# Kernel optimization log

Measured on AMD Instinct MI355X. Metric: run time of the kernel, lower is better.

## Reference

```python
import jax, jax.numpy as jnp
import numpy as np

N, D, H, C, E, I, L, B = 16000, 128, 2, 128, 256000, 512, 2, 64
NTYPES = 10


def setup_inputs() -> dict:
    key = jax.random.key(0)
    ks = jax.random.split(key, 20)
    s = 0.05
    inp = {
        'x': jax.random.normal(ks[0], (N, D), jnp.float32),
        'hetro_emb': jax.random.normal(ks[1], (NTYPES, D), jnp.float32) * s,
        'Wq': jax.random.normal(ks[2], (D, H * C), jnp.float32) * s,
        'bq': jnp.zeros((H * C,), jnp.float32),
        'Wk': jax.random.normal(ks[3], (D, H * C), jnp.float32) * s,
        'bk': jnp.zeros((H * C,), jnp.float32),
        'Wv': jax.random.normal(ks[4], (D, H * C), jnp.float32) * s,
        'bv': jnp.zeros((H * C,), jnp.float32),
        'We': jax.random.normal(ks[5], (D, H * C), jnp.float32) * s,
        'Wskip': jax.random.normal(ks[6], (D, C), jnp.float32) * s,
        'bskip': jnp.zeros((C,), jnp.float32),
        'ln_gamma': jnp.ones((L, D), jnp.float32),
        'ln_beta': jnp.zeros((L, D), jnp.float32),
        'ffn_w1': jax.random.normal(ks[7], (L, D, I), jnp.float32) * s,
        'ffn_b1': jnp.zeros((L, I), jnp.float32),
        'ffn_w2': jax.random.normal(ks[8], (L, I, D), jnp.float32) * s,
        'ffn_b2': jnp.zeros((L, D), jnp.float32),
        'edge_index': jax.random.randint(ks[9], (2, E), 0, N, jnp.int64),
        'edge_type': jax.random.randint(ks[10], (E,), 0, NTYPES, jnp.int64),
        'mask_idx': jax.random.randint(ks[11], (B,), 0, N, jnp.int64),
    }
    return inp


def _layer_norm(h, gamma, beta, eps=1e-6):
    mu = h.mean(-1, keepdims=True)
    var = ((h - mu) ** 2).mean(-1, keepdims=True)
    return (h - mu) * jax.lax.rsqrt(var + eps) * gamma + beta


def reference(x, hetro_emb, Wq, bq, Wk, bk, Wv, bv, We, Wskip, bskip,
              ln_gamma, ln_beta, ffn_w1, ffn_b1, ffn_w2, ffn_b2,
              edge_index, edge_type, mask_idx):
    src, dst = edge_index[0], edge_index[1]  # messages flow src(j) -> dst(i)
    edge_attr_raw = hetro_emb[edge_type]     # [E, D], computed once outside the layer loop
    scale = 1.0 / jnp.sqrt(jnp.asarray(C, x.dtype))

    h = x
    pre = h
    for l in range(L):
        # shared GRANConv weights across layers (same module appended n_gcn_layer times)
        q = (h @ Wq + bq).reshape(-1, H, C)
        k = (h @ Wk + bk).reshape(-1, H, C)
        v = (h @ Wv + bv).reshape(-1, H, C)
        eproj = (edge_attr_raw @ We).reshape(-1, H, C)  # [E, H, C]
        kj = k[src] + eproj                              # [E, H, C]
        logits = (q[dst] * kj).sum(-1) * scale           # [E, H]
        # segment softmax over destination nodes
        m = jax.ops.segment_max(logits, dst, num_segments=N)  # [N, H]
        a = jnp.exp(logits - m[dst])
        ssum = jax.ops.segment_sum(a, dst, num_segments=N)
        alpha = a / (ssum[dst] + 1e-16)                  # [E, H]
        msg = (v[src] + eproj) * alpha[..., None]        # [E, H, C]
        agg = jax.ops.segment_sum(msg, dst, num_segments=N)  # [N, H, C]
        out = agg.mean(1) + (h @ Wskip + bskip)          # concat=False -> head mean; root skip
        # residual + LN + FFN (no activation between the two FFN linears)
        hres = out + pre
        hln = _layer_norm(hres, ln_gamma[l], ln_beta[l])
        h = (hln @ ffn_w1[l] + ffn_b1[l]) @ ffn_w2[l] + ffn_b2[l]
        pre = h

    return h[mask_idx]  # [B, D]
```

## Files before the change

### kernel.cpp

```cpp
#include <hip/hip_runtime.h>
#include <hip/hip_bf16.h>
#include <math.h>

#define DD 128
#define QW 896
#define NB 125
#define BCAP 4096

typedef _Float16 f16x8 __attribute__((ext_vector_type(8)));
typedef _Float16 f16x4 __attribute__((ext_vector_type(4)));
typedef _Float16 f16x2 __attribute__((ext_vector_type(2)));
typedef float f32x4 __attribute__((ext_vector_type(4)));

__device__ __forceinline__ float fdot2f(f16x2 a, f16x2 b, float c) {
#if __has_builtin(__builtin_amdgcn_fdot2)
  return __builtin_amdgcn_fdot2(a, b, c, false);
#else
  return fmaf((float)a[0], (float)b[0], fmaf((float)a[1], (float)b[1], c));
#endif
}

__global__ __launch_bounds__(256) void csr_count(const int* __restrict__ edst,
                                                 int* __restrict__ bparts, int E) {
  __shared__ int h[NB];
  const int tid = threadIdx.x;
  if (tid < NB) h[tid] = 0;
  __syncthreads();
  const int e0 = blockIdx.x * 2048;
  for (int k = 0; k < 8; ++k) {
    int e = e0 + k * 256 + tid;
    if (e < E) atomicAdd(&h[edst[e] >> 7], 1);
  }
  __syncthreads();
  if (tid < 128) bparts[blockIdx.x * 128 + tid] = (tid < NB) ? h[tid] : 0;
}

__global__ __launch_bounds__(128) void csr_scan(const int* __restrict__ bparts, int nblk,
                                                int* __restrict__ bbase,
                                                int* __restrict__ bcursor,
                                                int* __restrict__ offs, int E, int Nn) {
  __shared__ int sc[128];
  const int tid = threadIdx.x;
  int s = 0;
  for (int b = 0; b < nblk; ++b) s += bparts[b * 128 + tid];
  sc[tid] = (tid < NB) ? s : 0;
  __syncthreads();
  for (int d = 1; d < 128; d <<= 1) {
    int t = (tid >= d) ? sc[tid - d] : 0;
    __syncthreads();
    sc[tid] += t;
    __syncthreads();
  }
  const int excl = tid ? sc[tid - 1] : 0;
  if (tid < NB) { bbase[tid] = excl; bcursor[tid] = excl; }
  if (tid == 0) { bbase[NB] = E; offs[Nn] = E; }
}

__global__ __launch_bounds__(256) void csr_scatter(const int* __restrict__ edst,
                                                   const int* __restrict__ esrc,
                                                   const int* __restrict__ etyp,
                                                   int* __restrict__ bcursor,
                                                   unsigned* __restrict__ ebuf, int E) {
  __shared__ int h[NB], cur[NB];
  const int tid = threadIdx.x;
  if (tid < NB) h[tid] = 0;
  __syncthreads();
  const int e0 = blockIdx.x * 2048;
  int dd[8];
  for (int k = 0; k < 8; ++k) {
    int e = e0 + k * 256 + tid;
    dd[k] = (e < E) ? edst[e] : -1;
    if (dd[k] >= 0) atomicAdd(&h[dd[k] >> 7], 1);
  }
  __syncthreads();
  if (tid < NB && h[tid]) cur[tid] = atomicAdd(&bcursor[tid], h[tid]);
  __syncthreads();
  for (int k = 0; k < 8; ++k) {
    int e = e0 + k * 256 + tid;
    if (dd[k] >= 0) {
      int pos = atomicAdd(&cur[dd[k] >> 7], 1);
      ebuf[pos] = (unsigned)esrc[e] | ((unsigned)etyp[e] << 14) |
                  ((unsigned)(dd[k] & 127) << 18);
    }
  }
}

__global__ __launch_bounds__(256) void csr_fine(const unsigned* __restrict__ ebuf,
                                                const int* __restrict__ bbase,
                                                unsigned* __restrict__ epk,
                                                int* __restrict__ offs,
                                                int* __restrict__ dparts) {
  __shared__ unsigned sed[BCAP];
  __shared__ unsigned sout[BCAP];
  __shared__ int fh[128], sc[128], fc[128], hb[64];
  const int b = blockIdx.x, tid = threadIdx.x;
  const int base = bbase[b], cnt = bbase[b + 1] - base;
  for (int idx = tid; idx < cnt; idx += 256) sed[idx] = ebuf[base + idx];
  if (tid < 128) fh[tid] = 0;
  if (tid < 64) hb[tid] = 0;
  __syncthreads();
  for (int idx = tid; idx < cnt; idx += 256) atomicAdd(&fh[(sed[idx] >> 18) & 127], 1);
  __syncthreads();
  if (tid < 128) sc[tid] = fh[tid];
  __syncthreads();
  for (int d = 1; d < 128; d <<= 1) {
    int t = (tid < 128 && tid >= d) ? sc[tid - d] : 0;
    __syncthreads();
    if (tid < 128) sc[tid] += t;
    __syncthreads();
  }
  if (tid < 128) {
    const int excl = tid ? sc[tid - 1] : 0;
    offs[b * 128 + tid] = base + excl;
    fc[tid] = excl;
    atomicAdd(&hb[min(fh[tid], 63)], 1);
  }
  __syncthreads();
  if (tid < 64) dparts[b * 64 + tid] = hb[tid];
  for (int idx = tid; idx < cnt; idx += 256) {
    const unsigned v = sed[idx];
    const int pos = atomicAdd(&fc[(v >> 18) & 127], 1);
    sout[pos] = (v & 0x3FFF) | (((v >> 14) & 0xF) << 18);
  }
  __syncthreads();
  for (int idx = tid; idx < cnt; idx += 256) epk[base + idx] = sout[idx];
}

__global__ __launch_bounds__(64) void deg_scan(const int* __restrict__ dparts, int nblk,
                                               int* __restrict__ dcur) {
  __shared__ int tot[64];
  const int t = threadIdx.x;
  int s = 0;
  for (int b = 0; b < nblk; ++b) s += dparts[b * 64 + t];
  tot[t] = s;
  __syncthreads();
  int acc = 0;
  for (int d = t + 1; d < 64; ++d) acc += tot[d];
  dcur[t] = acc;
}

__global__ __launch_bounds__(256) void deg_order(const int* __restrict__ offs,
                                                 int* __restrict__ dcur,
                                                 int* __restrict__ order, int Nn) {
  __shared__ int h[64], cbase[64];
  const int tid = threadIdx.x;
  const int i = blockIdx.x * 256 + tid;
  if (tid < 64) h[tid] = 0;
  __syncthreads();
  int bk = -1;
  if (i < Nn) {
    bk = min(offs[i + 1] - offs[i], 63);
    atomicAdd(&h[bk], 1);
  }
  __syncthreads();
  if (tid < 64) {
    const int c = h[tid];
    cbase[tid] = c ? atomicAdd(&dcur[tid], c) : 0;
    h[tid] = 0;
  }
  __syncthreads();
  if (bk >= 0) {
    const int pos = cbase[bk] + atomicAdd(&h[bk], 1);
    order[pos] = i;
  }
}

__global__ __launch_bounds__(256) void pp_cast(
    const float* __restrict__ Wq, const float* __restrict__ Wk,
    const float* __restrict__ Wv, const float* __restrict__ Wsk,
    const float* __restrict__ bq, const float* __restrict__ bk,
    const float* __restrict__ bv, const float* __restrict__ bsk,
    const float* __restrict__ hemb, const float* __restrict__ We,
    const float* __restrict__ x,
    const float* __restrict__ fw1, const float* __restrict__ fb1,
    const float* __restrict__ fw2, const float* __restrict__ fb2,
    _Float16* __restrict__ WcatT, float* __restrict__ Wcat, float* __restrict__ bcat,
    _Float16* __restrict__ epth, _Float16* __restrict__ xh,
    _Float16* __restrict__ fw1h, _Float16* __restrict__ fw2Th,
    float* __restrict__ bfv, float* __restrict__ bzero, int Nn, int nb0) {
  __shared__ _Float16 tile[64][65];
  if (blockIdx.x >= nb0) {
    const int tb = blockIdx.x - nb0;
    const int l = tb >> 4, r2 = tb & 15;
    const int k0 = (r2 >> 1) << 6, j0 = (r2 & 1) << 6;
    const size_t base = (size_t)l * 65536;
    const int tid = threadIdx.x;
    for (int idx = tid; idx < 4096; idx += 256) {
      int rr = idx >> 6, cc = idx & 63;
      tile[rr][cc] = (_Float16)fw2[base + (size_t)(k0 + rr) * 128 + j0 + cc];
    }
    __syncthreads();
    for (int idx = tid; idx < 4096; idx += 256) {
      int rr = idx >> 6, cc = idx & 63;
      fw2Th[base + (size_t)(j0 + rr) * 512 + k0 + cc] = tile[cc][rr];
    }
    return;
  }
  int t = blockIdx.x * 256 + threadIdx.x;
  if (t < 256) {
    int l = t >> 7, j = t & 127;
    const float* b1 = fb1 + l * 512;
    const float* w2 = fw2 + (size_t)l * 65536 + j;
    float s0 = fb2[l * 128 + j], s1 = 0.f, s2 = 0.f, s3 = 0.f;
    for (int k = 0; k < 512; k += 4) {
      s0 = fmaf(b1[k], w2[(size_t)k * 128], s0);
      s1 = fmaf(b1[k + 1], w2[(size_t)(k + 1) * 128], s1);
      s2 = fmaf(b1[k + 2], w2[(size_t)(k + 2) * 128], s2);
      s3 = fmaf(b1[k + 3], w2[(size_t)(k + 3) * 128], s3);
    }
    bfv[t] = ((s0 + s1) + (s2 + s3));
    return;
  }
  t -= 256;
  if (t < 2560) {
    int ty = t >> 8, col = t & 255;
    float s0 = 0.f, s1 = 0.f, s2 = 0.f, s3 = 0.f;
    const float* hr = hemb + ty * 128;
    for (int c = 0; c < 128; c += 4) {
      s0 = fmaf(hr[c], We[c * 256 + col], s0);
      s1 = fmaf(hr[c + 1], We[(c + 1) * 256 + col], s1);
      s2 = fmaf(hr[c + 2], We[(c + 2) * 256 + col], s2);
      s3 = fmaf(hr[c + 3], We[(c + 3) * 256 + col], s3);
    }
    epth[t] = (_Float16)((s0 + s1) + (s2 + s3));
    return;
  }
  t -= 2560;
  if (t < 114688) {
    int n = t >> 7, k = t & 127;
    float v;
    if (n < 256) v = Wq[k * 256 + n];
    else if (n < 512) v = Wk[k * 256 + (n - 256)];
    else if (n < 768) v = Wv[k * 256 + (n - 512)];
    else v = Wsk[k * 128 + (n - 768)];
    WcatT[t] = (_Float16)v;
    Wcat[k * 896 + n] = v;
    return;
  }
  t -= 114688;
  if (t < 896) {
    float v;
    if (t < 256) v = bq[t];
    else if (t < 512) v = bk[t - 256];
    else if (t < 768) v = bv[t - 512];
    else v = bsk[t - 768];
    bcat[t] = v;
    return;
  }
  t -= 896;
  if (t < 1024) { bzero[t] = 0.f; return; }
  t -= 1024;
  if (t < 16384) {
    float4 v0 = *reinterpret_cast<const float4*>(fw1 + (size_t)t * 8);
    float4 v1 = *reinterpret_cast<const float4*>(fw1 + (size_t)t * 8 + 4);
    f16x8 o;
    o[0] = (_Float16)v0.x; o[1] = (_Float16)v0.y; o[2] = (_Float16)v0.z; o[3] = (_Float16)v0.w;
    o[4] = (_Float16)v1.x; o[5] = (_Float16)v1.y; o[6] = (_Float16)v1.z; o[7] = (_Float16)v1.w;
    *reinterpret_cast<f16x8*>(fw1h + (size_t)t * 8) = o;
    return;
  }
  t -= 16384;
  if (t < Nn * 16) {
    float4 v0 = *reinterpret_cast<const float4*>(x + (size_t)t * 8);
    float4 v1 = *reinterpret_cast<const float4*>(x + (size_t)t * 8 + 4);
    f16x8 o;
    o[0] = (_Float16)v0.x; o[1] = (_Float16)v0.y; o[2] = (_Float16)v0.z; o[3] = (_Float16)v0.w;
    o[4] = (_Float16)v1.x; o[5] = (_Float16)v1.y; o[6] = (_Float16)v1.z; o[7] = (_Float16)v1.w;
    *reinterpret_cast<f16x8*>(xh + (size_t)t * 8) = o;
  }
}

__global__ __launch_bounds__(256) void pp_bmid(const float* __restrict__ bfv,
                                               const float* __restrict__ Wcat,
                                               const float* __restrict__ bcat,
                                               float* __restrict__ bmid) {
  int t = blockIdx.x * 256 + threadIdx.x;
  if (t >= 1024) return;
  if (t < 128) { bmid[t] = bfv[t]; return; }
  int n = t - 128;
  float s0 = bcat[n], s1 = 0.f, s2 = 0.f, s3 = 0.f;
  for (int c = 0; c < 128; c += 4) {
    s0 = fmaf(bfv[c], Wcat[c * 896 + n], s0);
    s1 = fmaf(bfv[c + 1], Wcat[(c + 1) * 896 + n], s1);
    s2 = fmaf(bfv[c + 2], Wcat[(c + 2) * 896 + n], s2);
    s3 = fmaf(bfv[c + 3], Wcat[(c + 3) * 896 + n], s3);
  }
  bmid[t] = ((s0 + s1) + (s2 + s3));
}

__global__ __launch_bounds__(256) void wf_gemm(const _Float16* __restrict__ fw1h,
                                               const _Float16* __restrict__ fw2Th,
                                               float* __restrict__ Wf,
                                               _Float16* __restrict__ Wfh,
                                               _Float16* __restrict__ BtMid0) {
  const int z = blockIdx.z;
  const _Float16* A = fw1h + z * 65536;
  const _Float16* Bt = fw2Th + z * 65536;
  const int tid = threadIdx.x;
  const int wid = tid >> 6, lane = tid & 63;
  const int wr = wid >> 1, wc = wid & 1;
  const int il = lane & 15, g = lane >> 4;
  const int row0 = wr * 64, col0 = wc * 64;
  const _Float16* Ap = A + (size_t)(row0 + il) * 512 + 8 * g;
  const _Float16* Bp = Bt + (size_t)(col0 + il) * 512 + 8 * g;
  f32x4 acc[4][4];
#pragma unroll
  for (int a = 0; a < 4; ++a)
#pragma unroll
    for (int b = 0; b < 4; ++b) acc[a][b] = (f32x4){0.f, 0.f, 0.f, 0.f};
  for (int k0 = 0; k0 < 512; k0 += 32) {
    f16x8 af[4], bf[4];
#pragma unroll
    for (int f = 0; f < 4; ++f) {
      af[f] = *reinterpret_cast<const f16x8*>(Ap + (size_t)(f * 16) * 512 + k0);
      bf[f] = *reinterpret_cast<const f16x8*>(Bp + (size_t)(f * 16) * 512 + k0);
    }
#pragma unroll
    for (int fi = 0; fi < 4; ++fi)
#pragma unroll
      for (int fj = 0; fj < 4; ++fj)
        acc[fi][fj] = __builtin_amdgcn_mfma_f32_16x16x32_f16(af[fi], bf[fj], acc[fi][fj], 0, 0, 0);
  }
#pragma unroll
  for (int fj = 0; fj < 4; ++fj) {
    const int col = col0 + fj * 16 + il;
#pragma unroll
    for (int fi = 0; fi < 4; ++fi) {
#pragma unroll
      for (int i = 0; i < 4; ++i) {
        const int row = row0 + fi * 16 + g * 4 + i;
        const float v = acc[fi][fj][i];
        Wf[z * 16384 + row * 128 + col] = v;
        if (z == 0) {
          Wfh[row * 128 + col] = (_Float16)v;
          BtMid0[col * 128 + row] = (_Float16)v;
        }
      }
    }
  }
}

template <bool HAS_CFH, bool HAS_CH, bool HAS_CHT>
__global__ __launch_bounds__(256) void gemm_tn_f16(const _Float16* __restrict__ A,
                                                   const _Float16* __restrict__ Bt,
                                                   const float* __restrict__ bias,
                                                   _Float16* __restrict__ Cfh, int NF,
                                                   _Float16* __restrict__ Ch, int choff, int ldh,
                                                   _Float16* __restrict__ ChT, int ldt,
                                                   int M, int N, int K) {
  __shared__ __align__(16) char smA[32768];
  __shared__ __align__(16) char smB[32768];
  const int tid = threadIdx.x;
  const int wid = tid >> 6, lane = tid & 63;
  const int wr = wid >> 1, wc = wid & 1;
  const int il = lane & 15, g = lane >> 4;
  const int row0 = blockIdx.y * 128;
  const int col0 = blockIdx.x * 128;
  {
    const f16x8* Ag = reinterpret_cast<const f16x8*>(A + (size_t)row0 * 128);
    const f16x8* Bg = reinterpret_cast<const f16x8*>(Bt + (size_t)col0 * 128);
#pragma unroll
    for (int it = 0; it < 8; ++it) {
      const int c = it * 256 + tid;
      const int r = c >> 4;
      const int off = r * 256 + (((c & 15) << 4) ^ ((r & 7) << 4));
      f16x8 va = Ag[c];
      f16x8 vb = Bg[c];
      *reinterpret_cast<f16x8*>(smA + off) = va;
      *reinterpret_cast<f16x8*>(smB + off) = vb;
    }
  }
  __syncthreads();
  f32x4 acc[4][4];
#pragma unroll
  for (int a = 0; a < 4; ++a)
#pragma unroll
    for (int b = 0; b < 4; ++b) acc[a][b] = (f32x4){0.f, 0.f, 0.f, 0.f};
#pragma unroll
  for (int ks = 0; ks < 4; ++ks) {
    const int kb = ks * 64 + g * 16;
    f16x8 af[4], bf[4];
#pragma unroll
    for (int f = 0; f < 4; ++f) {
      const int ra = wr * 64 + f * 16 + il;
      const int rb = wc * 64 + f * 16 + il;
      af[f] = *reinterpret_cast<const f16x8*>(smA + ra * 256 + (kb ^ ((ra & 7) << 4)));
      bf[f] = *reinterpret_cast<const f16x8*>(smB + rb * 256 + (kb ^ ((rb & 7) << 4)));
    }
#pragma unroll
    for (int fi = 0; fi < 4; ++fi)
#pragma unroll
      for (int fj = 0; fj < 4; ++fj)
        acc[fi][fj] = __builtin_amdgcn_mfma_f32_16x16x32_f16(bf[fj], af[fi], acc[fi][fj], 0, 0, 0);
  }
#pragma unroll
  for (int fi = 0; fi < 4; ++fi) {
    const int row = row0 + wr * 64 + fi * 16 + il;
#pragma unroll
    for (int fj = 0; fj < 4; ++fj) {
      const int col = col0 + wc * 64 + fj * 16 + g * 4;
      const float4 b4 = *reinterpret_cast<const float4*>(bias + col);
      f16x4 o;
      o[0] = (_Float16)(acc[fi][fj][0] + b4.x);
      o[1] = (_Float16)(acc[fi][fj][1] + b4.y);
      o[2] = (_Float16)(acc[fi][fj][2] + b4.z);
      o[3] = (_Float16)(acc[fi][fj][3] + b4.w);
      if constexpr (HAS_CFH) {
        if (col < NF) *reinterpret_cast<f16x4*>(&Cfh[(size_t)row * NF + col]) = o;
      }
      if constexpr (HAS_CH) {
        if (col >= choff) *reinterpret_cast<f16x4*>(&Ch[(size_t)row * ldh + (col - choff)]) = o;
      }
      if constexpr (HAS_CHT) {
#pragma unroll
        for (int i = 0; i < 4; ++i) ChT[(size_t)(col + i) * ldt + row] = o[i];
      }
    }
  }
}

__global__ __launch_bounds__(256) void node_attn_ln_kernel(
    const _Float16* __restrict__ QKVSh, const _Float16* __restrict__ epth,
    const _Float16* __restrict__ hpre,
    const int* __restrict__ offs, const unsigned* __restrict__ epk,
    const int* __restrict__ order,
    const float* __restrict__ gamma, const float* __restrict__ beta,
    _Float16* __restrict__ hlnh, int Nn) {
  __shared__ float sqe[4][2][10];
  __shared__ __align__(16) _Float16 elds[2560];
  const int tid = threadIdx.x;
  for (int t = tid; t < 1280; t += 256)
    reinterpret_cast<unsigned*>(elds)[t] = reinterpret_cast<const unsigned*>(epth)[t];
  __syncthreads();
  const int w = tid >> 6, lane = tid & 63;
  const int i = order[blockIdx.x * 4 + w];
  const int sub = lane >> 5;
  const int r = lane & 31;
  const int half = r >> 4;
  const int co = r << 3;
  const float scale = 0.08838834764831845f;
  f16x8 qh = *reinterpret_cast<const f16x8*>(QKVSh + (size_t)i * QW + co);
  const f16x2* q2 = reinterpret_cast<const f16x2*>(&qh);
#pragma unroll
  for (int ty = 0; ty < 10; ++ty) {
    f16x8 ev = *reinterpret_cast<const f16x8*>(elds + (ty << 8) + co);
    const f16x2* e2 = reinterpret_cast<const f16x2*>(&ev);
    float s = 0.f;
#pragma unroll
    for (int p2 = 0; p2 < 4; ++p2) s = fdot2f(q2[p2], e2[p2], s);
    s += __shfl_xor(s, 1); s += __shfl_xor(s, 2);
    s += __shfl_xor(s, 4); s += __shfl_xor(s, 8);
    if (lane < 32 && (r & 15) == 0) sqe[w][half][ty] = s * scale;
  }
  __threadfence_block();
  float m_me = -1e30f, s_me = 0.f;
  float acc[8] = {0.f};
  const int ebeg = offs[i], eend = offs[i + 1];
  if (ebeg < eend) {
    const int last = eend - 1;
    unsigned pk0 = epk[min(ebeg + sub, last)];
    unsigned pk1 = epk[min(ebeg + 2 + sub, last)];
    const _Float16* r0p = QKVSh + (size_t)(pk0 & 0x3FFFF) * QW;
    const _Float16* r1p = QKVSh + (size_t)(pk1 & 0x3FFFF) * QW;
    f16x8 kv0 = *reinterpret_cast<const f16x8*>(r0p + 256 + co);
    f16x8 vv0 = *reinterpret_cast<const f16x8*>(r0p + 512 + co);
    f16x8 kv1 = *reinterpret_cast<const f16x8*>(r1p + 256 + co);
    f16x8 vv1 = *reinterpret_cast<const f16x8*>(r1p + 512 + co);
    for (int j = ebeg; j < eend; j += 2) {
      f16x8 kc = kv0, vc = vv0;
      const unsigned pkc = pk0;
      kv0 = kv1; vv0 = vv1; pk0 = pk1;
      pk1 = epk[min(j + 4 + sub, last)];
      const _Float16* rp = QKVSh + (size_t)(pk1 & 0x3FFFF) * QW;
      kv1 = *reinterpret_cast<const f16x8*>(rp + 256 + co);
      vv1 = *reinterpret_cast<const f16x8*>(rp + 512 + co);
      const int tyc = pkc >> 18;
      const f16x2* k2 = reinterpret_cast<const f16x2*>(&kc);
      float d = 0.f;
#pragma unroll
      for (int p2 = 0; p2 < 4; ++p2) d = fdot2f(q2[p2], k2[p2], d);
      d += __shfl_xor(d, 1); d += __shfl_xor(d, 2);
      d += __shfl_xor(d, 4); d += __shfl_xor(d, 8);
      d = d * scale + sqe[w][half][tyc];
      float e;
      if (d > m_me + 8.f) {
        const float rr = __expf(m_me - d);
        s_me *= rr;
#pragma unroll
        for (int t = 0; t < 8; ++t) acc[t] *= rr;
        m_me = d;
        e = 1.f;
      } else {
        e = __expf(d - m_me);
      }
      if (j + sub >= eend) e = 0.f;
      s_me += e;
      f16x8 ec = *reinterpret_cast<const f16x8*>(elds + (tyc << 8) + co);
      f16x8 ve = vc + ec;
#pragma unroll
      for (int t = 0; t < 8; ++t) acc[t] = fmaf((float)ve[t], e, acc[t]);
    }
  }
  const float mo = __shfl_xor(m_me, 32);
  const float so = __shfl_xor(s_me, 32);
  const float mf = fmaxf(m_me, mo);
  const float sc_me = __expf(m_me - mf);
  const float sc_o = __expf(mo - mf);
  const float s_tot = s_me * sc_me + so * sc_o;
  const float invme = 1.f / (s_tot + 1e-16f);
  float g[8];
#pragma unroll
  for (int t = 0; t < 8; ++t) {
    const float ao = __shfl_xor(acc[t], 32);
    const float a = (acc[t] * sc_me + ao * sc_o) * invme;
    g[t] = 0.5f * (a + __shfl_xor(a, 16));
  }
  const int cm = (r & 15) << 3;
  f16x8 sk = *reinterpret_cast<const f16x8*>(QKVSh + (size_t)i * QW + 768 + cm);
  f16x8 pr = *reinterpret_cast<const f16x8*>(hpre + (size_t)i * DD + cm);
  float xv[8];
#pragma unroll
  for (int t = 0; t < 8; ++t) xv[t] = g[t] + (float)sk[t] + (float)pr[t];
  float sm = 0.f;
#pragma unroll
  for (int t = 0; t < 8; ++t) sm += xv[t];
  sm += __shfl_xor(sm, 1); sm += __shfl_xor(sm, 2);
  sm += __shfl_xor(sm, 4); sm += __shfl_xor(sm, 8);
  const float mu = sm * (1.f / 128.f);
  float dx[8], vvs = 0.f;
#pragma unroll
  for (int t = 0; t < 8; ++t) { dx[t] = xv[t] - mu; vvs += dx[t] * dx[t]; }
  vvs += __shfl_xor(vvs, 1); vvs += __shfl_xor(vvs, 2);
  vvs += __shfl_xor(vvs, 4); vvs += __shfl_xor(vvs, 8);
  const float rstd = rsqrtf(vvs * (1.f / 128.f) + 1e-6f);
  if (lane < 16) {
    float4 gm0 = *reinterpret_cast<const float4*>(gamma + cm);
    float4 gm1 = *reinterpret_cast<const float4*>(gamma + cm + 4);
    float4 bt0 = *reinterpret_cast<const float4*>(beta + cm);
    float4 bt1 = *reinterpret_cast<const float4*>(beta + cm + 4);
    f16x8 o;
    o[0] = (_Float16)(dx[0] * rstd * gm0.x + bt0.x);
    o[1] = (_Float16)(dx[1] * rstd * gm0.y + bt0.y);
    o[2] = (_Float16)(dx[2] * rstd * gm0.z + bt0.z);
    o[3] = (_Float16)(dx[3] * rstd * gm0.w + bt0.w);
    o[4] = (_Float16)(dx[4] * rstd * gm1.x + bt1.x);
    o[5] = (_Float16)(dx[5] * rstd * gm1.y + bt1.y);
    o[6] = (_Float16)(dx[6] * rstd * gm1.z + bt1.z);
    o[7] = (_Float16)(dx[7] * rstd * gm1.w + bt1.w);
    *reinterpret_cast<f16x8*>(hlnh + (size_t)i * DD + cm) = o;
  }
}

__global__ __launch_bounds__(128) void final_kernel(const _Float16* __restrict__ hlnh1,
                                                    const float* __restrict__ Wf,
                                                    const float* __restrict__ bfv,
                                                    const int* __restrict__ midx,
                                                    float* __restrict__ out) {
  __shared__ float rowv[128];
  const int b = blockIdx.x, j = threadIdx.x;
  const int row = midx[b];
  rowv[j] = (float)hlnh1[(size_t)row * DD + j];
  __syncthreads();
  const float* w1 = Wf + 16384 + j;
  float s = bfv[128 + j];
#pragma unroll 4
  for (int c = 0; c < 128; ++c) s = fmaf(rowv[c], w1[c * 128], s);
  out[b * DD + j] = s;
}

extern "C" void kernel_launch(void* const* d_in, const int* in_sizes, int n_in,
                              void* d_out, int out_size, void* d_ws, size_t ws_size,
                              hipStream_t stream) {
  const float* x    = (const float*)d_in[0];
  const float* hemb = (const float*)d_in[1];
  const float* Wq   = (const float*)d_in[2];
  const float* bq   = (const float*)d_in[3];
  const float* Wk   = (const float*)d_in[4];
  const float* bk   = (const float*)d_in[5];
  const float* Wv   = (const float*)d_in[6];
  const float* bv   = (const float*)d_in[7];
  const float* We   = (const float*)d_in[8];
  const float* Wsk  = (const float*)d_in[9];
  const float* bsk  = (const float*)d_in[10];
  const float* lng  = (const float*)d_in[11];
  const float* lnb  = (const float*)d_in[12];
  const float* fw1  = (const float*)d_in[13];
  const float* fb1  = (const float*)d_in[14];
  const float* fw2  = (const float*)d_in[15];
  const float* fb2  = (const float*)d_in[16];
  const int* eidx   = (const int*)d_in[17];
  const int* etyp   = (const int*)d_in[18];
  const int* midx   = (const int*)d_in[19];

  const int Nn = in_sizes[0] / DD;
  const int E = in_sizes[18];

  const int* esrc = eidx;
  const int* edst = eidx + E;

  char* p = (char*)d_ws;
  auto alloc = [&](size_t bytes) -> void* {
    void* r = (void*)p;
    p += (bytes + 255) & ~(size_t)255;
    return r;
  };
  _Float16* QKVSh = (_Float16*)alloc((size_t)Nn * QW * 2);
  _Float16* xh    = (_Float16*)alloc((size_t)Nn * DD * 2);
  _Float16* hln0  = (_Float16*)alloc((size_t)Nn * DD * 2);
  _Float16* hln1  = (_Float16*)alloc((size_t)Nn * DD * 2);
  _Float16* h1h   = (_Float16*)alloc((size_t)Nn * DD * 2);
  _Float16* WcatT = (_Float16*)alloc((size_t)QW * DD * 2);
  float*    Wcat  = (float*)alloc((size_t)DD * QW * 4);
  float*    bcat  = (float*)alloc(QW * 4);
  _Float16* epth  = (_Float16*)alloc(2560 * 2);
  _Float16* fw1h  = (_Float16*)alloc((size_t)2 * DD * 512 * 2);
  _Float16* fw2Th = (_Float16*)alloc((size_t)2 * DD * 512 * 2);
  float*    Wf    = (float*)alloc(2 * 128 * 128 * 4);
  _Float16* Wfh   = (_Float16*)alloc(128 * 128 * 2);
  float*    bfv   = (float*)alloc(256 * 4);
  float*    bzero = (float*)alloc(1024 * 4);
  _Float16* BtMid = (_Float16*)alloc((size_t)1024 * 128 * 2);
  float*    bmid  = (float*)alloc(1024 * 4);
  int* offs   = (int*)alloc((size_t)(Nn + 1) * 4);
  int* bbase  = (int*)alloc((NB + 1) * 4);
  int* bcursor= (int*)alloc((NB + 1) * 4);
  int* dcur   = (int*)alloc(64 * 4);
  int* order  = (int*)alloc((size_t)Nn * 4);
  const int nsblk = (E + 2047) / 2048;
  int* bparts = (int*)alloc((size_t)nsblk * 128 * 4);
  int* dparts = (int*)alloc((size_t)NB * 64 * 4);
  unsigned* ebuf = (unsigned*)alloc((size_t)E * 4);
  unsigned* epk  = (unsigned*)alloc((size_t)E * 4);

  csr_count<<<nsblk, 256, 0, stream>>>(edst, bparts, E);
  csr_scan<<<1, 128, 0, stream>>>(bparts, nsblk, bbase, bcursor, offs, E, Nn);
  csr_scatter<<<nsblk, 256, 0, stream>>>(edst, esrc, etyp, bcursor, ebuf, E);
  csr_fine<<<NB, 256, 0, stream>>>(ebuf, bbase, epk, offs, dparts);
  deg_scan<<<1, 64, 0, stream>>>(dparts, NB, dcur);
  deg_order<<<(Nn + 255) / 256, 256, 0, stream>>>(offs, dcur, order, Nn);

  const int pc_threads = 256 + 2560 + 114688 + 896 + 1024 + 16384 + Nn * 16;
  const int nb0 = (pc_threads + 255) / 256;
  pp_cast<<<nb0 + 32, 256, 0, stream>>>(
      Wq, Wk, Wv, Wsk, bq, bk, bv, bsk, hemb, We, x, fw1, fb1, fw2, fb2,
      WcatT, Wcat, bcat, epth, xh, fw1h, fw2Th, bfv, bzero, Nn, nb0);
  pp_bmid<<<4, 256, 0, stream>>>(bfv, Wcat, bcat, bmid);
  wf_gemm<<<dim3(1, 1, 2), 256, 0, stream>>>(fw1h, fw2Th, Wf, Wfh, BtMid);
  gemm_tn_f16<false, false, true><<<dim3(7, 1), 256, 0, stream>>>(
      Wfh, WcatT, bzero, nullptr, 0, nullptr, 0, 0, BtMid + 16384, 128, 128, 896, 128);

  gemm_tn_f16<false, true, false><<<dim3(QW / 128, Nn / 128), 256, 0, stream>>>(
      xh, WcatT, bcat, nullptr, 0, QKVSh, 0, QW, nullptr, 0, Nn, QW, DD);
  node_attn_ln_kernel<<<Nn / 4, 256, 0, stream>>>(QKVSh, epth, xh, offs, epk, order,
                                                  lng, lnb, hln0, Nn);
  gemm_tn_f16<true, true, false><<<dim3(1024 / 128, Nn / 128), 256, 0, stream>>>(
      hln0, BtMid, bmid, h1h, 128, QKVSh, 128, QW, nullptr, 0, Nn, 1024, DD);
  node_attn_ln_kernel<<<Nn / 4, 256, 0, stream>>>(QKVSh, epth, h1h, offs, epk, order,
                                                  lng + DD, lnb + DD, hln1, Nn);
  final_kernel<<<64, 128, 0, stream>>>(hln1, Wf, bfv, midx, (float*)d_out);
}
```

Baseline: 256.5 us.

## Store K/V in interleaved FP8 e4m3 to halve edge-gather traffic

The QKV GEMM epilogue now quantizes the K and V columns to FP8 e4m3 and packs them into a separate per-node 512-byte row, with K and V interleaved so each lane gets its slice in one 16-byte load. The attention kernel gathers these FP8 rows per edge instead of two f16 vectors, then converts them to float with the hardware packed FP8 conversion. The aim is to cut the random-gather memory traffic of the edge loop, which dominates. The cost is a large loss of precision in K and V (3 mantissa bits, small values flushed to zero), which may break the accuracy tolerance, plus extra conversion ALU work.

```diff
diff --git a/kernel.cpp b/kernel.cpp
--- a/kernel.cpp
+++ b/kernel.cpp
@@ -11,12 +11,40 @@
 typedef _Float16 f16x4 __attribute__((ext_vector_type(4)));
 typedef _Float16 f16x2 __attribute__((ext_vector_type(2)));
 typedef float f32x4 __attribute__((ext_vector_type(4)));
+typedef float f32x2 __attribute__((ext_vector_type(2)));
 
 __device__ __forceinline__ float fdot2f(f16x2 a, f16x2 b, float c) {
 #if __has_builtin(__builtin_amdgcn_fdot2)
   return __builtin_amdgcn_fdot2(a, b, c, false);
 #else
   return fmaf((float)a[0], (float)b[0], fmaf((float)a[1], (float)b[1], c));
+#endif
+}
+
+__device__ __forceinline__ unsigned e4m3b(float v) {
+  float a = fabsf(v);
+  unsigned s = (__float_as_uint(v) >> 24) & 0x80u;
+  if (!(a >= 0.015625f)) return s;
+  if (a > 448.f) a = 448.f;
+  unsigned u = __float_as_uint(a) + (1u << 19);
+  int e = (int)((u >> 23) & 255) - 120;
+  if (e > 15) return s | 0x7Eu;
+  return s | ((unsigned)e << 3) | ((u >> 20) & 7u);
+}
+__device__ __forceinline__ float e4m3f(unsigned b) {
+  unsigned em = b & 0x7Fu;
+  unsigned s = (b & 0x80u) << 24;
+  if (em == 0) return __uint_as_float(s);
+  return __uint_as_float(s | (((em >> 3) + 120u) << 23) | ((em & 7u) << 20));
+}
+template <bool HI>
+__device__ __forceinline__ f32x2 fp8x2f(unsigned w) {
+#if __has_builtin(__builtin_amdgcn_cvt_pk_f32_fp8)
+  return __builtin_amdgcn_cvt_pk_f32_fp8((int)w, HI);
+#else
+  unsigned h = HI ? (w >> 16) : w;
+  f32x2 r; r[0] = e4m3f(h & 255u); r[1] = e4m3f((h >> 8) & 255u);
+  return r;
 #endif
 }
 
@@ -340,13 +368,14 @@
   }
 }
 
-template <bool HAS_CFH, bool HAS_CH, bool HAS_CHT>
+template <bool HAS_CFH, bool HAS_CH, bool HAS_CHT, bool HAS_KVQ>
 __global__ __launch_bounds__(256) void gemm_tn_f16(const _Float16* __restrict__ A,
                                                    const _Float16* __restrict__ Bt,
                                                    const float* __restrict__ bias,
                                                    _Float16* __restrict__ Cfh, int NF,
                                                    _Float16* __restrict__ Ch, int choff, int ldh,
                                                    _Float16* __restrict__ ChT, int ldt,
+                                                   unsigned char* __restrict__ kvq,
                                                    int M, int N, int K) {
   __shared__ __align__(16) char smA[32768];
   __shared__ __align__(16) char smB[32768];
@@ -400,16 +429,26 @@
     for (int fj = 0; fj < 4; ++fj) {
       const int col = col0 + wc * 64 + fj * 16 + g * 4;
       const float4 b4 = *reinterpret_cast<const float4*>(bias + col);
+      float v0 = acc[fi][fj][0] + b4.x, v1 = acc[fi][fj][1] + b4.y;
+      float v2 = acc[fi][fj][2] + b4.z, v3 = acc[fi][fj][3] + b4.w;
       f16x4 o;
-      o[0] = (_Float16)(acc[fi][fj][0] + b4.x);
-      o[1] = (_Float16)(acc[fi][fj][1] + b4.y);
-      o[2] = (_Float16)(acc[fi][fj][2] + b4.z);
-      o[3] = (_Float16)(acc[fi][fj][3] + b4.w);
+      o[0] = (_Float16)v0; o[1] = (_Float16)v1; o[2] = (_Float16)v2; o[3] = (_Float16)v3;
+      const int ch = col - choff;
       if constexpr (HAS_CFH) {
         if (col < NF) *reinterpret_cast<f16x4*>(&Cfh[(size_t)row * NF + col]) = o;
       }
       if constexpr (HAS_CH) {
-        if (col >= choff) *reinterpret_cast<f16x4*>(&Ch[(size_t)row * ldh + (col - choff)]) = o;
+        const bool kvrange = HAS_KVQ && (ch >= 256 && ch < 768);
+        if (col >= choff && !kvrange)
+          *reinterpret_cast<f16x4*>(&Ch[(size_t)row * ldh + ch]) = o;
+      }
+      if constexpr (HAS_KVQ) {
+        if (ch >= 256 && ch < 768) {
+          const int c = (ch >= 512) ? (ch - 512) : (ch - 256);
+          const int boff = ((c >> 3) << 4) + (c & 7) + ((ch >= 512) ? 8 : 0);
+          unsigned pk = e4m3b(v0) | (e4m3b(v1) << 8) | (e4m3b(v2) << 16) | (e4m3b(v3) << 24);
+          *reinterpret_cast<unsigned*>(kvq + (size_t)row * 512 + boff) = pk;
+        }
       }
       if constexpr (HAS_CHT) {
 #pragma unroll
@@ -420,7 +459,8 @@
 }
 
 __global__ __launch_bounds__(256) void node_attn_ln_kernel(
-    const _Float16* __restrict__ QKVSh, const _Float16* __restrict__ epth,
+    const _Float16* __restrict__ QKVSh, const unsigned char* __restrict__ kvq,
+    const _Float16* __restrict__ epth,
     const _Float16* __restrict__ hpre,
     const int* __restrict__ offs, const unsigned* __restrict__ epk,
     const int* __restrict__ order,
@@ -441,6 +481,9 @@
   const float scale = 0.08838834764831845f;
   f16x8 qh = *reinterpret_cast<const f16x8*>(QKVSh + (size_t)i * QW + co);
   const f16x2* q2 = reinterpret_cast<const f16x2*>(&qh);
+  float qf[8];
+#pragma unroll
+  for (int t = 0; t < 8; ++t) qf[t] = (float)qh[t] * scale;
 #pragma unroll
   for (int ty = 0; ty < 10; ++ty) {
     f16x8 ev = *reinterpret_cast<const f16x8*>(elds + (ty << 8) + co);
@@ -460,28 +503,24 @@
     const int last = eend - 1;
     unsigned pk0 = epk[min(ebeg + sub, last)];
     unsigned pk1 = epk[min(ebeg + 2 + sub, last)];
-    const _Float16* r0p = QKVSh + (size_t)(pk0 & 0x3FFFF) * QW;
-    const _Float16* r1p = QKVSh + (size_t)(pk1 & 0x3FFFF) * QW;
-    f16x8 kv0 = *reinterpret_cast<const f16x8*>(r0p + 256 + co);
-    f16x8 vv0 = *reinterpret_cast<const f16x8*>(r0p + 512 + co);
-    f16x8 kv1 = *reinterpret_cast<const f16x8*>(r1p + 256 + co);
-    f16x8 vv1 = *reinterpret_cast<const f16x8*>(r1p + 512 + co);
+    uint4 kv0 = *reinterpret_cast<const uint4*>(kvq + (size_t)(pk0 & 0x3FFFF) * 512 + (r << 4));
+    uint4 kv1 = *reinterpret_cast<const uint4*>(kvq + (size_t)(pk1 & 0x3FFFF) * 512 + (r << 4));
     for (int j = ebeg; j < eend; j += 2) {
-      f16x8 kc = kv0, vc = vv0;
+      const uint4 cur = kv0;
       const unsigned pkc = pk0;
-      kv0 = kv1; vv0 = vv1; pk0 = pk1;
+      kv0 = kv1; pk0 = pk1;
       pk1 = epk[min(j + 4 + sub, last)];
-      const _Float16* rp = QKVSh + (size_t)(pk1 & 0x3FFFF) * QW;
-      kv1 = *reinterpret_cast<const f16x8*>(rp + 256 + co);
-      vv1 = *reinterpret_cast<const f16x8*>(rp + 512 + co);
+      kv1 = *reinterpret_cast<const uint4*>(kvq + (size_t)(pk1 & 0x3FFFF) * 512 + (r << 4));
       const int tyc = pkc >> 18;
-      const f16x2* k2 = reinterpret_cast<const f16x2*>(&kc);
-      float d = 0.f;
-#pragma unroll
-      for (int p2 = 0; p2 < 4; ++p2) d = fdot2f(q2[p2], k2[p2], d);
+      f32x2 k0 = fp8x2f<false>(cur.x), k1 = fp8x2f<true>(cur.x);
+      f32x2 k2 = fp8x2f<false>(cur.y), k3 = fp8x2f<true>(cur.y);
+      float d = qf[0] * k0[0];
+      d = fmaf(qf[1], k0[1], d); d = fmaf(qf[2], k1[0], d); d = fmaf(qf[3], k1[1], d);
+      d = fmaf(qf[4], k2[0], d); d = fmaf(qf[5], k2[1], d);
+      d = fmaf(qf[6], k3[0], d); d = fmaf(qf[7], k3[1], d);
       d += __shfl_xor(d, 1); d += __shfl_xor(d, 2);
       d += __shfl_xor(d, 4); d += __shfl_xor(d, 8);
-      d = d * scale + sqe[w][half][tyc];
+      d += sqe[w][half][tyc];
       float e;
       if (d > m_me + 8.f) {
         const float rr = __expf(m_me - d);
@@ -495,10 +534,15 @@
       }
       if (j + sub >= eend) e = 0.f;
       s_me += e;
+      f32x2 v0 = fp8x2f<false>(cur.z), v1 = fp8x2f<true>(cur.z);
+      f32x2 v2 = fp8x2f<false>(cur.w), v3 = fp8x2f<true>(cur.w);
       f16x8 ec = *reinterpret_cast<const f16x8*>(elds + (tyc << 8) + co);
-      f16x8 ve = vc + ec;
-#pragma unroll
-      for (int t = 0; t < 8; ++t) acc[t] = fmaf((float)ve[t], e, acc[t]);
+      acc[0] = fmaf(v0[0], e, acc[0]); acc[1] = fmaf(v0[1], e, acc[1]);
+      acc[2] = fmaf(v1[0], e, acc[2]); acc[3] = fmaf(v1[1], e, acc[3]);
+      acc[4] = fmaf(v2[0], e, acc[4]); acc[5] = fmaf(v2[1], e, acc[5]);
+      acc[6] = fmaf(v3[0], e, acc[6]); acc[7] = fmaf(v3[1], e, acc[7]);
+#pragma unroll
+      for (int t = 0; t < 8; ++t) acc[t] = fmaf((float)ec[t], e, acc[t]);
     }
   }
   const float mo = __shfl_xor(m_me, 32);
@@ -605,6 +649,7 @@
     return r;
   };
   _Float16* QKVSh = (_Float16*)alloc((size_t)Nn * QW * 2);
+  unsigned char* kvq = (unsigned char*)alloc((size_t)Nn * 512);
   _Float16* xh    = (_Float16*)alloc((size_t)Nn * DD * 2);
   _Float16* hln0  = (_Float16*)alloc((size_t)Nn * DD * 2);
   _Float16* hln1  = (_Float16*)alloc((size_t)Nn * DD * 2);
@@ -646,16 +691,17 @@
       WcatT, Wcat, bcat, epth, xh, fw1h, fw2Th, bfv, bzero, Nn, nb0);
   pp_bmid<<<4, 256, 0, stream>>>(bfv, Wcat, bcat, bmid);
   wf_gemm<<<dim3(1, 1, 2), 256, 0, stream>>>(fw1h, fw2Th, Wf, Wfh, BtMid);
-  gemm_tn_f16<false, false, true><<<dim3(7, 1), 256, 0, stream>>>(
-      Wfh, WcatT, bzero, nullptr, 0, nullptr, 0, 0, BtMid + 16384, 128, 128, 896, 128);
-
-  gemm_tn_f16<false, true, false><<<dim3(QW / 128, Nn / 128), 256, 0, stream>>>(
-      xh, WcatT, bcat, nullptr, 0, QKVSh, 0, QW, nullptr, 0, Nn, QW, DD);
-  node_attn_ln_kernel<<<Nn / 4, 256, 0, stream>>>(QKVSh, epth, xh, offs, epk, order,
+  gemm_tn_f16<false, false, true, false><<<dim3(7, 1), 256, 0, stream>>>(
+      Wfh, WcatT, bzero, nullptr, 0, nullptr, 0, 0, BtMid + 16384, 128, nullptr,
+      128, 896, 128);
+
+  gemm_tn_f16<false, true, false, true><<<dim3(QW / 128, Nn / 128), 256, 0, stream>>>(
+      xh, WcatT, bcat, nullptr, 0, QKVSh, 0, QW, nullptr, 0, kvq, Nn, QW, DD);
+  node_attn_ln_kernel<<<Nn / 4, 256, 0, stream>>>(QKVSh, kvq, epth, xh, offs, epk, order,
                                                   lng, lnb, hln0, Nn);
-  gemm_tn_f16<true, true, false><<<dim3(1024 / 128, Nn / 128), 256, 0, stream>>>(
-      hln0, BtMid, bmid, h1h, 128, QKVSh, 128, QW, nullptr, 0, Nn, 1024, DD);
-  node_attn_ln_kernel<<<Nn / 4, 256, 0, stream>>>(QKVSh, epth, h1h, offs, epk, order,
+  gemm_tn_f16<true, true, false, true><<<dim3(1024 / 128, Nn / 128), 256, 0, stream>>>(
+      hln0, BtMid, bmid, h1h, 128, QKVSh, 128, QW, nullptr, 0, kvq, Nn, 1024, DD);
+  node_attn_ln_kernel<<<Nn / 4, 256, 0, stream>>>(QKVSh, kvq, epth, h1h, offs, epk, order,
                                                   lng + DD, lnb + DD, hln1, Nn);
   final_kernel<<<64, 128, 0, stream>>>(hln1, Wf, bfv, midx, (float*)d_out);
 }
```

After: 245.4 us, median of 2. 1.05x faster.
